# Kernel tuning notes

Measured on AMD Instinct MI355X. Metric: run time of the kernel, lower is better.

## Reference

```python
import jax, jax.numpy as jnp
import numpy as np

B, L, D, H, MD = 8, 1024, 1024, 16, 6
DF = 4 * D
HD = D // H
EPS = 1e-5


def setup_inputs() -> dict:
    key = jax.random.key(0)
    ks = jax.random.split(key, 12)
    s = 0.02
    n = lambda k, shape: jax.random.normal(k, shape, dtype=jnp.float32) * s
    return {
        "x": jax.random.normal(ks[0], (B, L, D), dtype=jnp.float32),
        # attention sub-block
        "attn_norm_w": jnp.ones((D,), jnp.float32),
        "attn_norm_b": jnp.zeros((D,), jnp.float32),
        "in_proj_w": n(ks[1], (3 * D, D)),
        "in_proj_b": jnp.zeros((3 * D,), jnp.float32),
        "out_proj_w": n(ks[2], (D, D)),
        "out_proj_b": jnp.zeros((D,), jnp.float32),
        # ffn sub-block
        "ffn_norm_w": jnp.ones((D,), jnp.float32),
        "ffn_norm_b": jnp.zeros((D,), jnp.float32),
        "ffn_w1": n(ks[3], (DF, D)),
        "ffn_b1": jnp.zeros((DF,), jnp.float32),
        "ffn_w2": n(ks[4], (D, DF)),
        "ffn_b2": jnp.zeros((D,), jnp.float32),
        # router
        "rt_norm_w": jnp.ones((D,), jnp.float32),
        "rt_norm_b": jnp.zeros((D,), jnp.float32),
        "rt_w1": n(ks[5], (D, D)),
        "rt_b1": jnp.zeros((D,), jnp.float32),
        "rt_w2": n(ks[6], (MD, D)),
        "rt_b2": jnp.zeros((MD,), jnp.float32),
    }


def _layernorm(x, w, b):
    mu = jnp.mean(x, axis=-1, keepdims=True)
    var = jnp.mean(jnp.square(x - mu), axis=-1, keepdims=True)
    return (x - mu) * jax.lax.rsqrt(var + EPS) * w + b


def _mha(x, in_proj_w, in_proj_b, out_proj_w, out_proj_b):
    # packed qkv projection, torch nn.MultiheadAttention semantics (batch_first)
    qkv = x @ in_proj_w.T + in_proj_b                      # (B,L,3D)
    q, k, v = jnp.split(qkv, 3, axis=-1)
    def heads(t):
        return t.reshape(B, L, H, HD).transpose(0, 2, 1, 3)  # (B,H,L,HD)
    q, k, v = heads(q), heads(k), heads(v)
    scores = jnp.einsum("bhqd,bhkd->bhqk", q, k) / jnp.sqrt(jnp.float32(HD))
    attn = jax.nn.softmax(scores, axis=-1)
    ctx = jnp.einsum("bhqk,bhkd->bhqd", attn, v)           # (B,H,L,HD)
    ctx = ctx.transpose(0, 2, 1, 3).reshape(B, L, D)
    return ctx @ out_proj_w.T + out_proj_b


def _block(x, p):
    # pre-norm attention + residual
    a_in = _layernorm(x, p["attn_norm_w"], p["attn_norm_b"])
    x = x + _mha(a_in, p["in_proj_w"], p["in_proj_b"], p["out_proj_w"], p["out_proj_b"])
    # pre-norm FFN + residual (exact erf GELU, matching torch nn.GELU default)
    f_in = _layernorm(x, p["ffn_norm_w"], p["ffn_norm_b"])
    h = jax.nn.gelu(f_in @ p["ffn_w1"].T + p["ffn_b1"], approximate=False)
    x = x + h @ p["ffn_w2"].T + p["ffn_b2"]
    return x


def reference(x, attn_norm_w, attn_norm_b, in_proj_w, in_proj_b, out_proj_w,
              out_proj_b, ffn_norm_w, ffn_norm_b, ffn_w1, ffn_b1, ffn_w2,
              ffn_b2, rt_norm_w, rt_norm_b, rt_w1, rt_b1, rt_w2, rt_b2):
    p = dict(attn_norm_w=attn_norm_w, attn_norm_b=attn_norm_b,
             in_proj_w=in_proj_w, in_proj_b=in_proj_b,
             out_proj_w=out_proj_w, out_proj_b=out_proj_b,
             ffn_norm_w=ffn_norm_w, ffn_norm_b=ffn_norm_b,
             ffn_w1=ffn_w1, ffn_b1=ffn_b1, ffn_w2=ffn_w2, ffn_b2=ffn_b2)
    # router (eval mode: argmax, no Gumbel noise)
    r_in = _layernorm(x, rt_norm_w, rt_norm_b)
    h = jax.nn.gelu(r_in @ rt_w1.T + rt_b1, approximate=False)
    logits = h @ rt_w2.T + rt_b2                           # (B,L,MD)
    depths = jnp.argmax(logits, axis=-1) + 1               # (B,L) in [1,MD]
    cur = x
    for level in range(1, MD + 1):
        upd = _block(cur, p)
        cont = (depths >= level)[..., None]
        cur = jnp.where(cont, upd, cur)
    return cur, depths, logits
```

## Files before the change

kernel.cpp:

```cpp
#include <hip/hip_runtime.h>
#include <cstdint>
#include <cstddef>

typedef __bf16 bf16;
typedef bf16 bf16x8 __attribute__((ext_vector_type(8)));
typedef float f32x4 __attribute__((ext_vector_type(4)));

#define GAS __attribute__((address_space(1)))
#define LAS __attribute__((address_space(3)))

__device__ __forceinline__ void async_cp16(const bf16* g, bf16* l) {
  __builtin_amdgcn_global_load_lds((const GAS unsigned int*)g,
                                   (LAS unsigned int*)l, 16, 0, 0);
}

__device__ __forceinline__ float gelu_f(float x) {
  return 0.5f * x * (1.0f + erff(x * 0.70710678118654752440f));
}

__global__ void __launch_bounds__(256) f2b_kernel(const float* __restrict__ in,
                                                  bf16* __restrict__ out, int n) {
  int i = (blockIdx.x * 256 + threadIdx.x) * 4;
  if (i >= n) return;
  float4 v = *(const float4*)&in[i];
  union { uint2 u; bf16 e[4]; } o;
  o.e[0] = (bf16)v.x; o.e[1] = (bf16)v.y; o.e[2] = (bf16)v.z; o.e[3] = (bf16)v.w;
  *(uint2*)&out[i] = o.u;
}

__global__ void __launch_bounds__(256) split3_kernel(const float* __restrict__ in,
    bf16* __restrict__ oh, bf16* __restrict__ om, bf16* __restrict__ ol, int n) {
  int i = (blockIdx.x * 256 + threadIdx.x) * 4;
  if (i >= n) return;
  float4 v = *(const float4*)&in[i];
  float a[4] = {v.x, v.y, v.z, v.w};
  union { uint2 u; bf16 e[4]; } h, m, l;
#pragma unroll
  for (int j = 0; j < 4; j++) {
    h.e[j] = (bf16)a[j];
    float r = a[j] - (float)h.e[j];
    m.e[j] = (bf16)r;
    l.e[j] = (bf16)(r - (float)m.e[j]);
  }
  *(uint2*)&oh[i] = h.u;
  *(uint2*)&om[i] = m.u;
  *(uint2*)&ol[i] = l.u;
}

template<int SPLIT>
__global__ void __launch_bounds__(256) ln_kernel(const float* __restrict__ X,
    const float* __restrict__ w, const float* __restrict__ b,
    bf16* __restrict__ oh, bf16* __restrict__ om, bf16* __restrict__ ol) {
  const int row = blockIdx.x;
  const int tid = threadIdx.x;
  const float4 xv = *(const float4*)&X[(size_t)row * 1024 + tid * 4];
  float s1 = xv.x + xv.y + xv.z + xv.w;
  float s2 = xv.x * xv.x + xv.y * xv.y + xv.z * xv.z + xv.w * xv.w;
#pragma unroll
  for (int d = 1; d < 64; d <<= 1) {
    s1 += __shfl_xor(s1, d, 64);
    s2 += __shfl_xor(s2, d, 64);
  }
  __shared__ float red[8];
  if ((tid & 63) == 0) { red[tid >> 6] = s1; red[4 + (tid >> 6)] = s2; }
  __syncthreads();
  s1 = red[0] + red[1] + red[2] + red[3];
  s2 = red[4] + red[5] + red[6] + red[7];
  const float mu = s1 * (1.0f / 1024.0f);
  const float var = s2 * (1.0f / 1024.0f) - mu * mu;
  const float rs = rsqrtf(var + 1e-5f);
  const float4 wv = *(const float4*)&w[tid * 4];
  const float4 bv = *(const float4*)&b[tid * 4];
  float y[4] = {(xv.x - mu) * rs * wv.x + bv.x,
                (xv.y - mu) * rs * wv.y + bv.y,
                (xv.z - mu) * rs * wv.z + bv.z,
                (xv.w - mu) * rs * wv.w + bv.w};
  union { uint2 u; bf16 e[4]; } h;
#pragma unroll
  for (int j = 0; j < 4; j++) h.e[j] = (bf16)y[j];
  *(uint2*)&oh[(size_t)row * 1024 + tid * 4] = h.u;
  if (SPLIT == 3) {
    union { uint2 u; bf16 e[4]; } m, l;
#pragma unroll
    for (int j = 0; j < 4; j++) {
      float r = y[j] - (float)h.e[j];
      m.e[j] = (bf16)r;
      l.e[j] = (bf16)(r - (float)m.e[j]);
    }
    *(uint2*)&om[(size_t)row * 1024 + tid * 4] = m.u;
    *(uint2*)&ol[(size_t)row * 1024 + tid * 4] = l.u;
  }
}

template<int MODE>
__global__ void __launch_bounds__(256) gemm_nt(
    const bf16* __restrict__ A, const bf16* __restrict__ B,
    const float* __restrict__ bias, const float* __restrict__ Res,
    float* __restrict__ C32, bf16* __restrict__ Cb,
    const int* __restrict__ gate, int M, int N, int K, int level) {
  __shared__ bf16 As[128 * 32];
  __shared__ bf16 Bs[128 * 32];
  const int tid = threadIdx.x;
  const int w = tid >> 6, lane = tid & 63;
  const int lr = lane & 15, lq = lane >> 4;
  const int m0 = blockIdx.y * 128, n0 = blockIdx.x * 128;
  const int wm = (w >> 1) * 64, wn = (w & 1) * 64;

  f32x4 acc[4][4] = {};

  const bf16* ga = A + (size_t)(m0 + (tid >> 2)) * K + (tid & 3) * 8;
  const bf16* gb = B + (size_t)(n0 + (tid >> 2)) * K + (tid & 3) * 8;
  bf16* la = As + w * 512;
  bf16* lb = Bs + w * 512;
  const size_t step64 = (size_t)64 * K;

  for (int k0 = 0; k0 < K; k0 += 32) {
    __syncthreads();
    async_cp16(ga + k0, la);
    async_cp16(ga + step64 + k0, la + 2048);
    async_cp16(gb + k0, lb);
    async_cp16(gb + step64 + k0, lb + 2048);
    __syncthreads();
    bf16x8 af[4], bfr[4];
#pragma unroll
    for (int i = 0; i < 4; i++)
      af[i] = *(const bf16x8*)&As[(wm + i * 16 + lr) * 32 + lq * 8];
#pragma unroll
    for (int i = 0; i < 4; i++)
      bfr[i] = *(const bf16x8*)&Bs[(wn + i * 16 + lr) * 32 + lq * 8];
#pragma unroll
    for (int mi = 0; mi < 4; mi++)
#pragma unroll
      for (int ni = 0; ni < 4; ni++)
        acc[mi][ni] = __builtin_amdgcn_mfma_f32_16x16x32_bf16(
            af[mi], bfr[ni], acc[mi][ni], 0, 0, 0);
  }

#pragma unroll
  for (int mi = 0; mi < 4; mi++) {
    const int rbase = m0 + wm + mi * 16 + lq * 4;
#pragma unroll
    for (int ni = 0; ni < 4; ni++) {
      const int c = n0 + wn + ni * 16 + lr;
      float bv = 0.0f;
      if (MODE <= 3) bv = bias[c];
#pragma unroll
      for (int r = 0; r < 4; r++) {
        const size_t row = (size_t)(rbase + r);
        const float v = acc[mi][ni][r];
        if (MODE == 0) {
          Cb[row * N + c] = (bf16)(v + bv);
        } else if (MODE == 1) {
          C32[row * N + c] = Res[row * N + c] + v + bv;
        } else if (MODE == 2) {
          Cb[row * N + c] = (bf16)gelu_f(v + bv);
        } else if (MODE == 3) {
          if (gate[row] >= level) C32[row * N + c] = Res[row * N + c] + v + bv;
        } else if (MODE == 4) {
          C32[row * N + c] += v;
        } else {
          C32[row * N + c] = v;
        }
      }
    }
  }
}

__global__ void __launch_bounds__(256) gelu_bias_kernel(float* __restrict__ t,
    const float* __restrict__ bias, int n) {
  int i = (blockIdx.x * 256 + threadIdx.x) * 4;
  if (i >= n) return;
  float4 v = *(const float4*)&t[i];
  float4 bb = *(const float4*)&bias[i & 1023];
  v.x = gelu_f(v.x + bb.x);
  v.y = gelu_f(v.y + bb.y);
  v.z = gelu_f(v.z + bb.z);
  v.w = gelu_f(v.w + bb.w);
  *(float4*)&t[i] = v;
}

__global__ void __launch_bounds__(256) router_logits(const float* __restrict__ h,
    const float* __restrict__ w2, const float* __restrict__ b2,
    float* __restrict__ logits_out, float* __restrict__ depths_out,
    int* __restrict__ gate) {
  const int row = blockIdx.x * 4 + (threadIdx.x >> 6);
  const int lane = threadIdx.x & 63;
  const float* hr = h + (size_t)row * 1024;
  float part[6] = {0, 0, 0, 0, 0, 0};
  for (int kc = lane; kc < 256; kc += 64) {
    float4 hv = *(const float4*)&hr[kc * 4];
#pragma unroll
    for (int j = 0; j < 6; j++) {
      float4 wv = *(const float4*)&w2[j * 1024 + kc * 4];
      part[j] += hv.x * wv.x + hv.y * wv.y + hv.z * wv.z + hv.w * wv.w;
    }
  }
#pragma unroll
  for (int j = 0; j < 6; j++)
#pragma unroll
    for (int d = 1; d < 64; d <<= 1) part[j] += __shfl_xor(part[j], d, 64);
  if (lane == 0) {
    float best = -1e30f;
    int bi = 0;
#pragma unroll
    for (int j = 0; j < 6; j++) {
      const float v = part[j] + b2[j];
      logits_out[(size_t)row * 6 + j] = v;
      if (v > best) { best = v; bi = j; }
    }
    depths_out[row] = (float)(bi + 1);
    gate[row] = bi + 1;
  }
}

__global__ void __launch_bounds__(256) vtrans_kernel(const bf16* __restrict__ qkv,
                                                     bf16* __restrict__ vt) {
  __shared__ bf16 T[64 * 64];
  const int tid = threadIdx.x;
  const int tb = blockIdx.x & 15, bh = blockIdx.x >> 4;
  const int b = bh >> 4, h = bh & 15;
#pragma unroll
  for (int i = 0; i < 2; i++) {
    const int c = tid + i * 256;
    const int tok = c >> 3, hd8 = (c & 7) * 8;
    uint4 v = *(const uint4*)&qkv[((size_t)b * 1024 + tb * 64 + tok) * 3072 + 2048 + h * 64 + hd8];
    *(uint4*)&T[tok * 64 + (hd8 ^ ((tok & 7) << 3))] = v;
  }
  __syncthreads();
#pragma unroll
  for (int i = 0; i < 2; i++) {
    const int c = tid + i * 256;
    const int hd = c >> 3, t8 = (c & 7) * 8;
    union { uint4 u; bf16 e[8]; } o;
#pragma unroll
    for (int j = 0; j < 8; j++)
      o.e[j] = T[(t8 + j) * 64 + (hd ^ (j << 3))];
    *(uint4*)&vt[((size_t)bh * 64 + hd) * 1024 + tb * 64 + t8] = o.u;
  }
}

__global__ void __launch_bounds__(256) attn_kernel(const bf16* __restrict__ qkv,
                                                   const bf16* __restrict__ vtg,
                                                   bf16* __restrict__ ctx) {
  __shared__ bf16 Qs[64 * 72];
  __shared__ bf16 Ks[64 * 72];
  __shared__ bf16 Vt[64 * 72];
  __shared__ bf16 Ps[64 * 72];
  const int tid = threadIdx.x;
  const int w = tid >> 6, lane = tid & 63;
  const int lr = lane & 15, lq = lane >> 4;
  const int blk = blockIdx.x;
  const int bh = (blk & 7) | ((blk >> 7) << 3);
  const int qt = (blk >> 3) & 15;
  const int b = bh >> 4, h = bh & 15;
  const size_t rowbase = (size_t)b * 1024;
  const int hcol = h * 64;
  const size_t vbase = (size_t)bh * 65536;

#pragma unroll
  for (int i = 0; i < 2; i++) {
    const int c = tid + i * 256;
    const int r = c >> 3, k8 = (c & 7) * 8;
    uint4 v = *(const uint4*)&qkv[(rowbase + qt * 64 + r) * 3072 + hcol + k8];
    *(uint4*)&Qs[r * 72 + k8] = v;
  }
  __syncthreads();
  bf16x8 aq[2];
#pragma unroll
  for (int hs = 0; hs < 2; hs++)
    aq[hs] = *(const bf16x8*)&Qs[(w * 16 + lr) * 72 + hs * 32 + lq * 8];

  float lsum[4] = {0.0f, 0.0f, 0.0f, 0.0f};
  f32x4 o[4];
#pragma unroll
  for (int i = 0; i < 4; i++) o[i] = (f32x4)0.0f;

  const int Sw = ((w * 4 + lq) & 7) << 3;
  const int Sr = ((w * 4 + (lr >> 2)) & 7) << 3;

  for (int kb = 0; kb < 16; kb++) {
    __syncthreads();
#pragma unroll
    for (int i = 0; i < 2; i++) {
      const int c = tid + i * 256;
      const int r = c >> 3, k8 = (c & 7) * 8;
      uint4 v = *(const uint4*)&qkv[(rowbase + kb * 64 + r) * 3072 + 1024 + hcol + k8];
      *(uint4*)&Ks[r * 72 + k8] = v;
    }
#pragma unroll
    for (int i = 0; i < 2; i++) {
      const int c = tid + i * 256;
      const int hd = c >> 3, t8 = (c & 7) * 8;
      uint4 v = *(const uint4*)&vtg[vbase + (size_t)hd * 1024 + kb * 64 + t8];
      *(uint4*)&Vt[hd * 72 + (t8 ^ (hd & 56))] = v;
    }
    __syncthreads();

    f32x4 s[4];
#pragma unroll
    for (int kf = 0; kf < 4; kf++) {
      f32x4 sa = (f32x4)0.0f;
#pragma unroll
      for (int hs = 0; hs < 2; hs++) {
        bf16x8 bk = *(const bf16x8*)&Ks[(kf * 16 + lr) * 72 + hs * 32 + lq * 8];
        sa = __builtin_amdgcn_mfma_f32_16x16x32_bf16(aq[hs], bk, sa, 0, 0, 0);
      }
      s[kf] = sa;
    }

#pragma unroll
    for (int kf = 0; kf < 4; kf++) {
#pragma unroll
      for (int r = 0; r < 4; r++) {
        const float p = __expf(s[kf][r] * 0.125f);
        lsum[r] += p;
        const int row = w * 16 + lq * 4 + r;
        Ps[row * 72 + ((kf * 16 + lr) ^ Sw)] = (bf16)p;
      }
    }

    bf16x8 ap[2];
#pragma unroll
    for (int ks = 0; ks < 2; ks++)
      ap[ks] = *(const bf16x8*)&Ps[(w * 16 + lr) * 72 + ((ks * 32 + lq * 8) ^ Sr)];
#pragma unroll
    for (int hf = 0; hf < 4; hf++) {
      const int vrow = hf * 16 + lr;
#pragma unroll
      for (int ks = 0; ks < 2; ks++) {
        bf16x8 bv = *(const bf16x8*)&Vt[vrow * 72 + ((ks * 32 + lq * 8) ^ (vrow & 56))];
        o[hf] = __builtin_amdgcn_mfma_f32_16x16x32_bf16(ap[ks], bv, o[hf], 0, 0, 0);
      }
    }
  }

#pragma unroll
  for (int r = 0; r < 4; r++) {
#pragma unroll
    for (int d = 1; d < 16; d <<= 1) lsum[r] += __shfl_xor(lsum[r], d, 64);
  }

#pragma unroll
  for (int r = 0; r < 4; r++) {
    const float inv = 1.0f / lsum[r];
    const size_t row = rowbase + qt * 64 + w * 16 + lq * 4 + r;
#pragma unroll
    for (int hf = 0; hf < 4; hf++)
      ctx[row * 1024 + hcol + hf * 16 + lr] = (bf16)(o[hf][r] * inv);
  }
}

extern "C" void kernel_launch(void* const* d_in, const int* in_sizes, int n_in,
                              void* d_out, int out_size, void* d_ws, size_t ws_size,
                              hipStream_t stream) {
  (void)in_sizes; (void)n_in; (void)out_size; (void)ws_size;
  const float* x    = (const float*)d_in[0];
  const float* a_nw = (const float*)d_in[1];
  const float* a_nb = (const float*)d_in[2];
  const float* in_w = (const float*)d_in[3];
  const float* in_b = (const float*)d_in[4];
  const float* o_w  = (const float*)d_in[5];
  const float* o_b  = (const float*)d_in[6];
  const float* f_nw = (const float*)d_in[7];
  const float* f_nb = (const float*)d_in[8];
  const float* w1   = (const float*)d_in[9];
  const float* b1   = (const float*)d_in[10];
  const float* w2   = (const float*)d_in[11];
  const float* b2   = (const float*)d_in[12];
  const float* r_nw = (const float*)d_in[13];
  const float* r_nb = (const float*)d_in[14];
  const float* rw1  = (const float*)d_in[15];
  const float* rb1  = (const float*)d_in[16];
  const float* rw2  = (const float*)d_in[17];
  const float* rb2  = (const float*)d_in[18];

  float* cur    = (float*)d_out;
  float* depths = cur + 8388608;
  float* logits = depths + 8192;

  char* ws = (char*)d_ws;
  bf16* wb_in  = (bf16*)(ws + 0);
  bf16* wb_out = (bf16*)(ws + 6291456);
  bf16* wb_f1  = (bf16*)(ws + 8388608);
  bf16* wb_f2  = (bf16*)(ws + 16777216);
  bf16* r1h    = (bf16*)(ws + 25165824);
  bf16* r1m    = (bf16*)(ws + 27262976);
  bf16* r1l    = (bf16*)(ws + 29360128);
  bf16* Abuf   = (bf16*)(ws + 31457280);
  bf16* Bbuf   = (bf16*)(ws + 48234496);
  bf16* Big    = (bf16*)(ws + 65011712);
  float* Tmp   = (float*)(ws + 132120576);
  bf16* VtG    = (bf16*)(ws + 132120576);
  int*  gate   = (int*)(ws + 165675008);

  hipMemcpyAsync(cur, x, (size_t)8388608 * 4, hipMemcpyDeviceToDevice, stream);

  f2b_kernel<<<3072, 256, 0, stream>>>(in_w, wb_in, 3145728);
  f2b_kernel<<<1024, 256, 0, stream>>>(o_w, wb_out, 1048576);
  f2b_kernel<<<4096, 256, 0, stream>>>(w1, wb_f1, 4194304);
  f2b_kernel<<<4096, 256, 0, stream>>>(w2, wb_f2, 4194304);
  split3_kernel<<<1024, 256, 0, stream>>>(rw1, r1h, r1m, r1l, 1048576);

  ln_kernel<3><<<8192, 256, 0, stream>>>(x, r_nw, r_nb, Abuf, Bbuf, Big);
  dim3 g1k(8, 64);
  gemm_nt<5><<<g1k, 256, 0, stream>>>(Abuf, r1h, nullptr, nullptr, Tmp, nullptr, nullptr, 8192, 1024, 1024, 0);
  gemm_nt<4><<<g1k, 256, 0, stream>>>(Abuf, r1m, nullptr, nullptr, Tmp, nullptr, nullptr, 8192, 1024, 1024, 0);
  gemm_nt<4><<<g1k, 256, 0, stream>>>(Bbuf, r1h, nullptr, nullptr, Tmp, nullptr, nullptr, 8192, 1024, 1024, 0);
  gemm_nt<4><<<g1k, 256, 0, stream>>>(Abuf, r1l, nullptr, nullptr, Tmp, nullptr, nullptr, 8192, 1024, 1024, 0);
  gemm_nt<4><<<g1k, 256, 0, stream>>>(Bbuf, r1m, nullptr, nullptr, Tmp, nullptr, nullptr, 8192, 1024, 1024, 0);
  gemm_nt<4><<<g1k, 256, 0, stream>>>(Big,  r1h, nullptr, nullptr, Tmp, nullptr, nullptr, 8192, 1024, 1024, 0);
  gelu_bias_kernel<<<8192, 256, 0, stream>>>(Tmp, rb1, 8388608);
  router_logits<<<2048, 256, 0, stream>>>(Tmp, rw2, rb2, logits, depths, gate);

  for (int level = 1; level <= 6; level++) {
    ln_kernel<1><<<8192, 256, 0, stream>>>(cur, a_nw, a_nb, Abuf, nullptr, nullptr);
    gemm_nt<0><<<dim3(24, 64), 256, 0, stream>>>(Abuf, wb_in, in_b, nullptr, nullptr, Big, nullptr, 8192, 3072, 1024, 0);
    vtrans_kernel<<<2048, 256, 0, stream>>>(Big, VtG);
    attn_kernel<<<2048, 256, 0, stream>>>(Big, VtG, Bbuf);
    gemm_nt<1><<<dim3(8, 64), 256, 0, stream>>>(Bbuf, wb_out, o_b, cur, Tmp, nullptr, nullptr, 8192, 1024, 1024, 0);
    ln_kernel<1><<<8192, 256, 0, stream>>>(Tmp, f_nw, f_nb, Abuf, nullptr, nullptr);
    gemm_nt<2><<<dim3(32, 64), 256, 0, stream>>>(Abuf, wb_f1, b1, nullptr, nullptr, Big, nullptr, 8192, 4096, 1024, 0);
    gemm_nt<3><<<dim3(8, 64), 256, 0, stream>>>(Big, wb_f2, b2, Tmp, cur, nullptr, gate, 8192, 1024, 4096, level);
  }
}
```

Baseline: 3.016 ms.

## Fuse split-precision router GEMMs into one kernel and swizzle GEMM tile order

Replaces the six sequential split-precision router GEMM launches with a single kernel that loads the hi/mid/lo splits of both operands into shared memory and accumulates all six cross products in registers. This avoids the repeated global reads of the activations and weights and the repeated read-modify-write of the fp32 output. Separately, all GEMMs now remap block indices so groups of 8 row tiles share a column tile, aiming for better L2 reuse. The fused kernel uses three times the shared memory per block, which may lower occupancy, and the swizzle assumes the row-tile count is a multiple of 8.

```diff
diff --git a/kernel.cpp b/kernel.cpp
--- a/kernel.cpp
+++ b/kernel.cpp
@@ -92,6 +92,13 @@
   }
 }
 
+__device__ __forceinline__ void swizzle_mn(int gx, int& m0, int& n0) {
+  const int id = blockIdx.y * gx + blockIdx.x;
+  const int k8 = id & 7, t = id >> 3;
+  n0 = (t % gx) * 128;
+  m0 = ((t / gx) * 8 + k8) * 128;
+}
+
 template<int MODE>
 __global__ void __launch_bounds__(256) gemm_nt(
     const bf16* __restrict__ A, const bf16* __restrict__ B,
@@ -103,7 +110,8 @@
   const int tid = threadIdx.x;
   const int w = tid >> 6, lane = tid & 63;
   const int lr = lane & 15, lq = lane >> 4;
-  const int m0 = blockIdx.y * 128, n0 = blockIdx.x * 128;
+  int m0, n0;
+  swizzle_mn(gridDim.x, m0, n0);
   const int wm = (w >> 1) * 64, wn = (w & 1) * 64;
 
   f32x4 acc[4][4] = {};
@@ -162,6 +170,73 @@
           C32[row * N + c] = v;
         }
       }
+    }
+  }
+}
+
+__global__ void __launch_bounds__(256) gemm_router(
+    const bf16* __restrict__ Ah, const bf16* __restrict__ Am, const bf16* __restrict__ Al,
+    const bf16* __restrict__ Bh, const bf16* __restrict__ Bm, const bf16* __restrict__ Bl,
+    float* __restrict__ C32) {
+  __shared__ bf16 As[3][128 * 32];
+  __shared__ bf16 Bs[3][128 * 32];
+  const int tid = threadIdx.x;
+  const int w = tid >> 6, lane = tid & 63;
+  const int lr = lane & 15, lq = lane >> 4;
+  int m0, n0;
+  swizzle_mn(gridDim.x, m0, n0);
+  const int wm = (w >> 1) * 64, wn = (w & 1) * 64;
+  const int K = 1024;
+
+  f32x4 acc[4][4] = {};
+
+  const size_t aoff = (size_t)(m0 + (tid >> 2)) * K + (tid & 3) * 8;
+  const size_t boff = (size_t)(n0 + (tid >> 2)) * K + (tid & 3) * 8;
+  const bf16* gA[3] = {Ah + aoff, Am + aoff, Al + aoff};
+  const bf16* gB[3] = {Bh + boff, Bm + boff, Bl + boff};
+  const int lo = w * 512;
+  const size_t step64 = (size_t)64 * K;
+
+  const int cA[6] = {0, 0, 1, 1, 0, 2};
+  const int cB[6] = {0, 1, 0, 1, 2, 0};
+
+  for (int k0 = 0; k0 < K; k0 += 32) {
+    __syncthreads();
+#pragma unroll
+    for (int j = 0; j < 3; j++) {
+      async_cp16(gA[j] + k0, As[j] + lo);
+      async_cp16(gA[j] + step64 + k0, As[j] + lo + 2048);
+      async_cp16(gB[j] + k0, Bs[j] + lo);
+      async_cp16(gB[j] + step64 + k0, Bs[j] + lo + 2048);
+    }
+    __syncthreads();
+#pragma unroll
+    for (int c = 0; c < 6; c++) {
+      bf16x8 af[4], bfr[4];
+#pragma unroll
+      for (int i = 0; i < 4; i++)
+        af[i] = *(const bf16x8*)&As[cA[c]][(wm + i * 16 + lr) * 32 + lq * 8];
+#pragma unroll
+      for (int i = 0; i < 4; i++)
+        bfr[i] = *(const bf16x8*)&Bs[cB[c]][(wn + i * 16 + lr) * 32 + lq * 8];
+#pragma unroll
+      for (int mi = 0; mi < 4; mi++)
+#pragma unroll
+        for (int ni = 0; ni < 4; ni++)
+          acc[mi][ni] = __builtin_amdgcn_mfma_f32_16x16x32_bf16(
+              af[mi], bfr[ni], acc[mi][ni], 0, 0, 0);
+    }
+  }
+
+#pragma unroll
+  for (int mi = 0; mi < 4; mi++) {
+    const int rbase = m0 + wm + mi * 16 + lq * 4;
+#pragma unroll
+    for (int ni = 0; ni < 4; ni++) {
+      const int c = n0 + wn + ni * 16 + lr;
+#pragma unroll
+      for (int r = 0; r < 4; r++)
+        C32[(size_t)(rbase + r) * 1024 + c] = acc[mi][ni][r];
     }
   }
 }
@@ -402,13 +477,7 @@
   split3_kernel<<<1024, 256, 0, stream>>>(rw1, r1h, r1m, r1l, 1048576);
 
   ln_kernel<3><<<8192, 256, 0, stream>>>(x, r_nw, r_nb, Abuf, Bbuf, Big);
-  dim3 g1k(8, 64);
-  gemm_nt<5><<<g1k, 256, 0, stream>>>(Abuf, r1h, nullptr, nullptr, Tmp, nullptr, nullptr, 8192, 1024, 1024, 0);
-  gemm_nt<4><<<g1k, 256, 0, stream>>>(Abuf, r1m, nullptr, nullptr, Tmp, nullptr, nullptr, 8192, 1024, 1024, 0);
-  gemm_nt<4><<<g1k, 256, 0, stream>>>(Bbuf, r1h, nullptr, nullptr, Tmp, nullptr, nullptr, 8192, 1024, 1024, 0);
-  gemm_nt<4><<<g1k, 256, 0, stream>>>(Abuf, r1l, nullptr, nullptr, Tmp, nullptr, nullptr, 8192, 1024, 1024, 0);
-  gemm_nt<4><<<g1k, 256, 0, stream>>>(Bbuf, r1m, nullptr, nullptr, Tmp, nullptr, nullptr, 8192, 1024, 1024, 0);
-  gemm_nt<4><<<g1k, 256, 0, stream>>>(Big,  r1h, nullptr, nullptr, Tmp, nullptr, nullptr, 8192, 1024, 1024, 0);
+  gemm_router<<<dim3(8, 64), 256, 0, stream>>>(Abuf, Bbuf, Big, r1h, r1m, r1l, Tmp);
   gelu_bias_kernel<<<8192, 256, 0, stream>>>(Tmp, rb1, 8388608);
   router_logits<<<2048, 256, 0, stream>>>(Tmp, rw2, rb2, logits, depths, gate);
 
```

Result: faster. 2.820 ms (-6.5%).
